# Kernel tuning notes

Measured on AMD Instinct MI355X. Metric: run time of the kernel, lower is better.

Reference implementation:

```python
import jax, jax.numpy as jnp
import numpy as np

EPS = 1e-8  # torch F.cosine_similarity denominator clamp


def setup_inputs() -> dict:
    key = jax.random.key(0)
    k1, k2 = jax.random.split(key)
    N, D = 8192, 256
    return {
        "output1": jax.random.normal(k1, (N, D), dtype=jnp.float32),
        "output2": jax.random.normal(k2, (N, D), dtype=jnp.float32),
    }


def reference(output1, output2):
    N = output2.shape[0]
    # cosine similarity matrix via normalize + GEMM, with torch's eps clamp
    n1 = jnp.linalg.norm(output1, axis=-1, keepdims=True)  # [N,1]
    n2 = jnp.linalg.norm(output2, axis=-1, keepdims=True)  # [N,1]
    dots = output1 @ output2.T  # [N,N]
    denom = jnp.maximum(n1 * n2.T, EPS)
    cos = dots / denom
    # subtract tiny diagonal as in original
    cos = cos - jnp.eye(N, dtype=cos.dtype) * 1e-12
    # cross entropy with labels = arange(N)
    logZ = jax.nn.logsumexp(cos, axis=-1)  # [N]
    diag = jnp.diagonal(cos)  # logits at true label i
    loss = jnp.mean(logZ - diag)
    return loss
```

## Files before the change

### kernel.cpp

```cpp
#include <hip/hip_runtime.h>
#include <hip/hip_bf16.h>

#define N 8192
#define D 256
#define SP 8
#define NCHK 16

typedef __bf16 bf16x8 __attribute__((ext_vector_type(8)));
typedef float f32x4 __attribute__((ext_vector_type(4)));

static __device__ __forceinline__ unsigned short f2bf(float x) {
    union { float f; unsigned int u; } c; c.f = x;
    unsigned int r = (c.u + 0x7fffu + ((c.u >> 16) & 1u)) >> 16;
    return (unsigned short)r;
}

static __device__ __forceinline__ void gll16(const void* g, void* l) {
    __builtin_amdgcn_global_load_lds(
        (const __attribute__((address_space(1))) void*)g,
        (__attribute__((address_space(3))) void*)l, 16, 0, 0);
}

#define WAIT_VM0  asm volatile("s_waitcnt vmcnt(0)" ::: "memory")
#define WAIT_LG0  asm volatile("s_waitcnt lgkmcnt(0)" ::: "memory")
#define SBAR      __builtin_amdgcn_s_barrier()
#define SCHED0    __builtin_amdgcn_sched_barrier(0)

__global__ __launch_bounds__(256) void conv_k(const float* __restrict__ o1,
                                              const float* __restrict__ o2,
                                              unsigned char* __restrict__ a_bf,
                                              unsigned char* __restrict__ b_bf,
                                              float* __restrict__ diag) {
    const int wid = threadIdx.x >> 6, lane = threadIdx.x & 63;
    const int r = blockIdx.x * 4 + wid;
    const float4* p1 = (const float4*)(o1 + (size_t)r * D);
    const float4* p2 = (const float4*)(o2 + (size_t)r * D);
    float4 v1 = p1[lane], v2 = p2[lane];
    float s1 = v1.x*v1.x + v1.y*v1.y + v1.z*v1.z + v1.w*v1.w;
    float s2 = v2.x*v2.x + v2.y*v2.y + v2.z*v2.z + v2.w*v2.w;
    float sd = v1.x*v2.x + v1.y*v2.y + v1.z*v2.z + v1.w*v2.w;
    #pragma unroll
    for (int m = 1; m < 64; m <<= 1) {
        s1 += __shfl_xor(s1, m);
        s2 += __shfl_xor(s2, m);
        sd += __shfl_xor(sd, m);
    }
    float i1 = 1.0f / sqrtf(s1);
    float i2 = 1.0f / sqrtf(s2);
    if (lane == 0) diag[r] = sd * i1 * i2;

    {
        unsigned int lo = (unsigned int)f2bf(v1.x * i1) | ((unsigned int)f2bf(v1.y * i1) << 16);
        unsigned int hi = (unsigned int)f2bf(v1.z * i1) | ((unsigned int)f2bf(v1.w * i1) << 16);
        uint2 q; q.x = lo; q.y = hi;
        *(uint2*)(a_bf + (size_t)r * 512 + lane * 8) = q;
    }
    {
        unsigned int lo = (unsigned int)f2bf(v2.x * i2) | ((unsigned int)f2bf(v2.y * i2) << 16);
        unsigned int hi = (unsigned int)f2bf(v2.z * i2) | ((unsigned int)f2bf(v2.w * i2) << 16);
        int c  = lane >> 1;
        int cs = c ^ (r & 31);
        uint2 q; q.x = lo; q.y = hi;
        *(uint2*)(b_bf + (size_t)r * 512 + cs * 16 + (lane & 1) * 8) = q;
    }
}

__global__ __launch_bounds__(256, 2) void gemm8(const unsigned char* __restrict__ a_bf,
                                                const unsigned char* __restrict__ b_bf,
                                                float* __restrict__ s_part) {
    __shared__ __align__(16) unsigned char bls[2][64 * 512];
    __shared__ float red[2][128];

    const int tid = threadIdx.x;
    const int lane = tid & 63, wid = tid >> 6;
    const int wr = wid >> 1, wc = wid & 1;
    const int l15 = lane & 15, lk = lane >> 4;
    const int bid = blockIdx.x;
    const int sp = bid & 7, rb = bid >> 3;

    const unsigned char* aG = a_bf + (size_t)rb * (128 * 512);
    const unsigned char* bG = b_bf + (size_t)sp * ((size_t)1024 * 512);

    bf16x8 af[4][8];
    #pragma unroll
    for (int mr = 0; mr < 4; ++mr)
        #pragma unroll
        for (int ks = 0; ks < 8; ++ks)
            af[mr][ks] = *(const bf16x8*)(aG + (size_t)(wr * 64 + mr * 16 + l15) * 512
                                             + ks * 64 + lk * 16);

    #pragma unroll
    for (int it = 0; it < 8; ++it) {
        int x = it * 4096 + tid * 16;
        gll16(bG + x, &bls[0][x]);
    }

    float srow[4][4];
    #pragma unroll
    for (int mr = 0; mr < 4; ++mr)
        #pragma unroll
        for (int rg = 0; rg < 4; ++rg) srow[mr][rg] = 0.f;

    const unsigned char* cur = bls[0];
    unsigned char* nxt = bls[1];

    #pragma unroll 1
    for (int p = 0; p < NCHK; ++p) {
        WAIT_VM0;
        SCHED0;
        SBAR;

        if (p < NCHK - 1) {
            const unsigned char* src = bG + (size_t)(p + 1) * 32768;
            #pragma unroll
            for (int it = 0; it < 8; ++it) {
                int x = it * 4096 + tid * 16;
                gll16(src + x, nxt + x);
            }
        }

        f32x4 acc[4][2];
        #pragma unroll
        for (int mr = 0; mr < 4; ++mr)
            #pragma unroll
            for (int nc = 0; nc < 2; ++nc)
                acc[mr][nc] = (f32x4){0.f, 0.f, 0.f, 0.f};

        __builtin_amdgcn_s_setprio(1);
        #pragma unroll
        for (int ks = 0; ks < 8; ++ks) {
            bf16x8 bb[2];
            #pragma unroll
            for (int nc = 0; nc < 2; ++nc) {
                const int col = wc * 32 + nc * 16 + l15;
                const int cs = (ks * 4 + lk) ^ (col & 31);
                bb[nc] = *(const bf16x8*)(cur + col * 512 + cs * 16);
            }
            #pragma unroll
            for (int nc = 0; nc < 2; ++nc)
                #pragma unroll
                for (int mr = 0; mr < 4; ++mr)
                    acc[mr][nc] = __builtin_amdgcn_mfma_f32_16x16x32_bf16(
                        af[mr][ks], bb[nc], acc[mr][nc], 0, 0, 0);
        }
        __builtin_amdgcn_s_setprio(0);
        WAIT_LG0;
        SCHED0;

        #pragma unroll
        for (int mr = 0; mr < 4; ++mr)
            #pragma unroll
            for (int rg = 0; rg < 4; ++rg)
                srow[mr][rg] += __expf(acc[mr][0][rg]) + __expf(acc[mr][1][rg]);

        unsigned char* t = (unsigned char*)cur; cur = nxt; nxt = t;
    }

    #pragma unroll
    for (int mr = 0; mr < 4; ++mr)
        #pragma unroll
        for (int rg = 0; rg < 4; ++rg) {
            float v = srow[mr][rg];
            v += __shfl_xor(v, 1);
            v += __shfl_xor(v, 2);
            v += __shfl_xor(v, 4);
            v += __shfl_xor(v, 8);
            srow[mr][rg] = v;
        }
    if (l15 == 0) {
        #pragma unroll
        for (int mr = 0; mr < 4; ++mr)
            #pragma unroll
            for (int rg = 0; rg < 4; ++rg)
                red[wc][wr * 64 + mr * 16 + lk * 4 + rg] = srow[mr][rg];
    }
    __syncthreads();
    if (tid < 128) {
        s_part[(size_t)sp * N + rb * 128 + tid] = red[0][tid] + red[1][tid];
    }
}

__global__ __launch_bounds__(128) void rowloss3(const float* __restrict__ s_part,
                                                const float* __restrict__ diag,
                                                float* __restrict__ partial) {
    const int t = threadIdx.x, rb = blockIdx.x;
    float s = 0.f;
    #pragma unroll
    for (int sp = 0; sp < SP; ++sp)
        s += s_part[(size_t)sp * N + rb * 128 + t];
    float loss = logf(s) - diag[rb * 128 + t];
    #pragma unroll
    for (int m = 1; m < 64; m <<= 1) loss += __shfl_xor(loss, m);
    __shared__ float redl[2];
    if ((t & 63) == 0) redl[t >> 6] = loss;
    __syncthreads();
    if (t == 0) partial[rb] = redl[0] + redl[1];
}

__global__ __launch_bounds__(64) void final_k(const float* __restrict__ partial,
                                              float* __restrict__ out) {
    const int t = threadIdx.x;
    float v = partial[t];
    #pragma unroll
    for (int m = 1; m < 64; m <<= 1) v += __shfl_xor(v, m);
    if (t == 0) out[0] = v / (float)N;
}

extern "C" void kernel_launch(void* const* d_in, const int* in_sizes, int n_in,
                              void* d_out, int out_size, void* d_ws, size_t ws_size,
                              hipStream_t stream) {
    const float* o1 = (const float*)d_in[0];
    const float* o2 = (const float*)d_in[1];

    unsigned char* w = (unsigned char*)d_ws;
    unsigned char* a_bf = w;
    unsigned char* b_bf = w + (size_t)4 * 1024 * 1024;
    float* diag    = (float*)(w + (size_t)8 * 1024 * 1024);
    float* s_part  = diag + N;
    float* partial = s_part + (size_t)SP * N;

    conv_k<<<N / 4, 256, 0, stream>>>(o1, o2, a_bf, b_bf, diag);
    gemm8<<<512, 256, 0, stream>>>(a_bf, b_bf, s_part);
    rowloss3<<<N / 128, 128, 0, stream>>>(s_part, diag, partial);
    final_k<<<1, 64, 0, stream>>>(partial, (float*)d_out);
}
```

Before: 53.54 us.

## Give each wave private double-buffered B staging and fold log2e into A

The GEMM now has each wave stream its own 16-column B chunks into a private LDS double buffer, waiting with vmcnt(8). This removes the block-wide barrier per chunk, and each wave computes one column group over 32 smaller chunks. The A operand is prescaled by log2(e) in the conversion kernel, so the softmax sum can use exp2f instead of __expf. In exchange, B tiles that two waves used to share are now loaded twice from global memory, which roughly doubles B traffic through L2. Per-chunk MFMA work is also smaller, which exposes more load latency.

```diff
diff --git a/kernel.cpp b/kernel.cpp
--- a/kernel.cpp
+++ b/kernel.cpp
@@ -4,7 +4,8 @@
 #define N 8192
 #define D 256
 #define SP 8
-#define NCHK 16
+#define NCHK 32
+#define LOG2E 1.44269504088896f
 
 typedef __bf16 bf16x8 __attribute__((ext_vector_type(8)));
 typedef float f32x4 __attribute__((ext_vector_type(4)));
@@ -21,9 +22,9 @@
         (__attribute__((address_space(3))) void*)l, 16, 0, 0);
 }
 
+#define WAIT_VM8  asm volatile("s_waitcnt vmcnt(8)" ::: "memory")
 #define WAIT_VM0  asm volatile("s_waitcnt vmcnt(0)" ::: "memory")
 #define WAIT_LG0  asm volatile("s_waitcnt lgkmcnt(0)" ::: "memory")
-#define SBAR      __builtin_amdgcn_s_barrier()
 #define SCHED0    __builtin_amdgcn_sched_barrier(0)
 
 __global__ __launch_bounds__(256) void conv_k(const float* __restrict__ o1,
@@ -49,9 +50,10 @@
     float i2 = 1.0f / sqrtf(s2);
     if (lane == 0) diag[r] = sd * i1 * i2;
 
+    float a_sc = i1 * LOG2E;
     {
-        unsigned int lo = (unsigned int)f2bf(v1.x * i1) | ((unsigned int)f2bf(v1.y * i1) << 16);
-        unsigned int hi = (unsigned int)f2bf(v1.z * i1) | ((unsigned int)f2bf(v1.w * i1) << 16);
+        unsigned int lo = (unsigned int)f2bf(v1.x * a_sc) | ((unsigned int)f2bf(v1.y * a_sc) << 16);
+        unsigned int hi = (unsigned int)f2bf(v1.z * a_sc) | ((unsigned int)f2bf(v1.w * a_sc) << 16);
         uint2 q; q.x = lo; q.y = hi;
         *(uint2*)(a_bf + (size_t)r * 512 + lane * 8) = q;
     }
@@ -65,96 +67,89 @@
     }
 }
 
-__global__ __launch_bounds__(256, 2) void gemm8(const unsigned char* __restrict__ a_bf,
+__global__ __launch_bounds__(256, 2) void gemm9(const unsigned char* __restrict__ a_bf,
                                                 const unsigned char* __restrict__ b_bf,
                                                 float* __restrict__ s_part) {
-    __shared__ __align__(16) unsigned char bls[2][64 * 512];
+    __shared__ __align__(16) unsigned char bls[4][16384];
     __shared__ float red[2][128];
 
     const int tid = threadIdx.x;
     const int lane = tid & 63, wid = tid >> 6;
-    const int wr = wid >> 1, wc = wid & 1;
+    const int wrow = wid >> 1, ch = wid & 1;
     const int l15 = lane & 15, lk = lane >> 4;
     const int bid = blockIdx.x;
-    const int sp = bid & 7, rb = bid >> 3;
-
-    const unsigned char* aG = a_bf + (size_t)rb * (128 * 512);
-    const unsigned char* bG = b_bf + (size_t)sp * ((size_t)1024 * 512);
+    const int panel = bid & 7, rb = bid >> 3;
+
+    const unsigned char* aG = a_bf + (size_t)(rb * 128 + wrow * 64) * 512;
+    const unsigned char* bG = b_bf + (size_t)(panel * 1024 + ch * 512) * 512;
+    unsigned char* myl = bls[wid];
 
     bf16x8 af[4][8];
     #pragma unroll
     for (int mr = 0; mr < 4; ++mr)
         #pragma unroll
         for (int ks = 0; ks < 8; ++ks)
-            af[mr][ks] = *(const bf16x8*)(aG + (size_t)(wr * 64 + mr * 16 + l15) * 512
+            af[mr][ks] = *(const bf16x8*)(aG + (size_t)(mr * 16 + l15) * 512
                                              + ks * 64 + lk * 16);
 
-    #pragma unroll
-    for (int it = 0; it < 8; ++it) {
-        int x = it * 4096 + tid * 16;
-        gll16(bG + x, &bls[0][x]);
-    }
+#define STAGE(c, b)                                                             \
+    {                                                                           \
+        const unsigned char* src_ = bG + (size_t)(c) * 8192;                    \
+        unsigned char* dst_ = myl + (b) * 8192;                                 \
+        _Pragma("unroll")                                                       \
+        for (int it = 0; it < 8; ++it) {                                        \
+            int x_ = it * 1024 + lane * 16;                                     \
+            gll16(src_ + x_, dst_ + x_);                                        \
+        }                                                                       \
+    }
+
+    STAGE(0, 0);
+    STAGE(1, 1);
 
     float srow[4][4];
     #pragma unroll
     for (int mr = 0; mr < 4; ++mr)
         #pragma unroll
         for (int rg = 0; rg < 4; ++rg) srow[mr][rg] = 0.f;
-
-    const unsigned char* cur = bls[0];
-    unsigned char* nxt = bls[1];
 
     #pragma unroll 1
     for (int p = 0; p < NCHK; ++p) {
-        WAIT_VM0;
+        if (p < NCHK - 1) { WAIT_VM8; } else { WAIT_VM0; }
         SCHED0;
-        SBAR;
-
-        if (p < NCHK - 1) {
-            const unsigned char* src = bG + (size_t)(p + 1) * 32768;
-            #pragma unroll
-            for (int it = 0; it < 8; ++it) {
-                int x = it * 4096 + tid * 16;
-                gll16(src + x, nxt + x);
-            }
+
+        const unsigned char* cb = myl + (p & 1) * 8192;
+        const int key = (p & 1) * 16 + l15;
+        bf16x8 bb[8];
+        #pragma unroll
+        for (int ks = 0; ks < 8; ++ks) {
+            const int cs = (ks * 4 + lk) ^ key;
+            bb[ks] = *(const bf16x8*)(cb + l15 * 512 + cs * 16);
         }
-
-        f32x4 acc[4][2];
-        #pragma unroll
-        for (int mr = 0; mr < 4; ++mr)
-            #pragma unroll
-            for (int nc = 0; nc < 2; ++nc)
-                acc[mr][nc] = (f32x4){0.f, 0.f, 0.f, 0.f};
-
-        __builtin_amdgcn_s_setprio(1);
-        #pragma unroll
-        for (int ks = 0; ks < 8; ++ks) {
-            bf16x8 bb[2];
-            #pragma unroll
-            for (int nc = 0; nc < 2; ++nc) {
-                const int col = wc * 32 + nc * 16 + l15;
-                const int cs = (ks * 4 + lk) ^ (col & 31);
-                bb[nc] = *(const bf16x8*)(cur + col * 512 + cs * 16);
-            }
-            #pragma unroll
-            for (int nc = 0; nc < 2; ++nc)
-                #pragma unroll
-                for (int mr = 0; mr < 4; ++mr)
-                    acc[mr][nc] = __builtin_amdgcn_mfma_f32_16x16x32_bf16(
-                        af[mr][ks], bb[nc], acc[mr][nc], 0, 0, 0);
-        }
-        __builtin_amdgcn_s_setprio(0);
         WAIT_LG0;
         SCHED0;
+        if (p + 2 < NCHK) STAGE(p + 2, p & 1);
+        SCHED0;
+
+        f32x4 acc[4];
+        #pragma unroll
+        for (int mr = 0; mr < 4; ++mr) acc[mr] = (f32x4){0.f, 0.f, 0.f, 0.f};
+
+        __builtin_amdgcn_s_setprio(1);
+        #pragma unroll
+        for (int ks = 0; ks < 8; ++ks)
+            #pragma unroll
+            for (int mr = 0; mr < 4; ++mr)
+                acc[mr] = __builtin_amdgcn_mfma_f32_16x16x32_bf16(
+                    af[mr][ks], bb[ks], acc[mr], 0, 0, 0);
+        __builtin_amdgcn_s_setprio(0);
 
         #pragma unroll
         for (int mr = 0; mr < 4; ++mr)
             #pragma unroll
             for (int rg = 0; rg < 4; ++rg)
-                srow[mr][rg] += __expf(acc[mr][0][rg]) + __expf(acc[mr][1][rg]);
-
-        unsigned char* t = (unsigned char*)cur; cur = nxt; nxt = t;
-    }
+                srow[mr][rg] += exp2f(acc[mr][rg]);
+    }
+#undef STAGE
 
     #pragma unroll
     for (int mr = 0; mr < 4; ++mr)
@@ -172,11 +167,11 @@
         for (int mr = 0; mr < 4; ++mr)
             #pragma unroll
             for (int rg = 0; rg < 4; ++rg)
-                red[wc][wr * 64 + mr * 16 + lk * 4 + rg] = srow[mr][rg];
+                red[ch][wrow * 64 + mr * 16 + lk * 4 + rg] = srow[mr][rg];
     }
     __syncthreads();
     if (tid < 128) {
-        s_part[(size_t)sp * N + rb * 128 + tid] = red[0][tid] + red[1][tid];
+        s_part[(size_t)panel * N + rb * 128 + tid] = red[0][tid] + red[1][tid];
     }
 }
 
@@ -220,7 +215,7 @@
     float* partial = s_part + (size_t)SP * N;
 
     conv_k<<<N / 4, 256, 0, stream>>>(o1, o2, a_bf, b_bf, diag);
-    gemm8<<<512, 256, 0, stream>>>(a_bf, b_bf, s_part);
+    gemm9<<<512, 256, 0, stream>>>(a_bf, b_bf, s_part);
     rowloss3<<<N / 128, 128, 0, stream>>>(s_part, diag, partial);
     final_k<<<1, 64, 0, stream>>>(partial, (float*)d_out);
 }
```

Measured after the change: 62.57 us. 1.17x slower.

## Switch similarity GEMM from bf16 to fp8 scaled MFMA with log2e folding

Applied to the files above, without the earlier changes.

Normalized rows are now quantized to fp8 instead of bf16. The GEMM uses the 16x16x128 f8f6f4 scaled MFMA with neutral scales, which halves operand bytes and LDS traffic and cuts the number of MFMA issues. The LDS swizzle is reworked for the 256-byte rows. The log2(e) factor is folded into the A operand so the epilogue can use exp2f instead of expf. The cost is fp8 precision in the cosine logits, which may shift the loss beyond tolerance.

```diff
diff --git a/kernel.cpp b/kernel.cpp
--- a/kernel.cpp
+++ b/kernel.cpp
@@ -5,15 +5,11 @@
 #define D 256
 #define SP 8
 #define NCHK 16
-
-typedef __bf16 bf16x8 __attribute__((ext_vector_type(8)));
+#define LOG2E 1.44269504088896f
+
+typedef int   i32x4 __attribute__((ext_vector_type(4)));
+typedef int   i32x8 __attribute__((ext_vector_type(8)));
 typedef float f32x4 __attribute__((ext_vector_type(4)));
-
-static __device__ __forceinline__ unsigned short f2bf(float x) {
-    union { float f; unsigned int u; } c; c.f = x;
-    unsigned int r = (c.u + 0x7fffu + ((c.u >> 16) & 1u)) >> 16;
-    return (unsigned short)r;
-}
 
 static __device__ __forceinline__ void gll16(const void* g, void* l) {
     __builtin_amdgcn_global_load_lds(
@@ -28,8 +24,8 @@
 
 __global__ __launch_bounds__(256) void conv_k(const float* __restrict__ o1,
                                               const float* __restrict__ o2,
-                                              unsigned char* __restrict__ a_bf,
-                                              unsigned char* __restrict__ b_bf,
+                                              unsigned char* __restrict__ a8,
+                                              unsigned char* __restrict__ b8,
                                               float* __restrict__ diag) {
     const int wid = threadIdx.x >> 6, lane = threadIdx.x & 63;
     const int r = blockIdx.x * 4 + wid;
@@ -49,26 +45,25 @@
     float i2 = 1.0f / sqrtf(s2);
     if (lane == 0) diag[r] = sd * i1 * i2;
 
+    float a_sc = i1 * LOG2E;
     {
-        unsigned int lo = (unsigned int)f2bf(v1.x * i1) | ((unsigned int)f2bf(v1.y * i1) << 16);
-        unsigned int hi = (unsigned int)f2bf(v1.z * i1) | ((unsigned int)f2bf(v1.w * i1) << 16);
-        uint2 q; q.x = lo; q.y = hi;
-        *(uint2*)(a_bf + (size_t)r * 512 + lane * 8) = q;
+        int pa = __builtin_amdgcn_cvt_pk_fp8_f32(v1.x * a_sc, v1.y * a_sc, 0, false);
+        pa     = __builtin_amdgcn_cvt_pk_fp8_f32(v1.z * a_sc, v1.w * a_sc, pa, true);
+        *(int*)(a8 + (size_t)r * 256 + lane * 4) = pa;
     }
     {
-        unsigned int lo = (unsigned int)f2bf(v2.x * i2) | ((unsigned int)f2bf(v2.y * i2) << 16);
-        unsigned int hi = (unsigned int)f2bf(v2.z * i2) | ((unsigned int)f2bf(v2.w * i2) << 16);
-        int c  = lane >> 1;
-        int cs = c ^ (r & 31);
-        uint2 q; q.x = lo; q.y = hi;
-        *(uint2*)(b_bf + (size_t)r * 512 + cs * 16 + (lane & 1) * 8) = q;
-    }
-}
-
-__global__ __launch_bounds__(256, 2) void gemm8(const unsigned char* __restrict__ a_bf,
-                                                const unsigned char* __restrict__ b_bf,
-                                                float* __restrict__ s_part) {
-    __shared__ __align__(16) unsigned char bls[2][64 * 512];
+        int pb = __builtin_amdgcn_cvt_pk_fp8_f32(v2.x * i2, v2.y * i2, 0, false);
+        pb     = __builtin_amdgcn_cvt_pk_fp8_f32(v2.z * i2, v2.w * i2, pb, true);
+        int c  = lane >> 2;
+        int cs = c ^ (r & 15);
+        *(int*)(b8 + (size_t)r * 256 + cs * 16 + (lane & 3) * 4) = pb;
+    }
+}
+
+__global__ __launch_bounds__(256, 2) void gemm11(const unsigned char* __restrict__ a8,
+                                                 const unsigned char* __restrict__ b8,
+                                                 float* __restrict__ s_part) {
+    __shared__ __align__(16) unsigned char bls[2][16384];
     __shared__ float red[2][128];
 
     const int tid = threadIdx.x;
@@ -76,21 +71,21 @@
     const int wr = wid >> 1, wc = wid & 1;
     const int l15 = lane & 15, lk = lane >> 4;
     const int bid = blockIdx.x;
-    const int sp = bid & 7, rb = bid >> 3;
-
-    const unsigned char* aG = a_bf + (size_t)rb * (128 * 512);
-    const unsigned char* bG = b_bf + (size_t)sp * ((size_t)1024 * 512);
-
-    bf16x8 af[4][8];
+    const int panel = bid & 7, rb = bid >> 3;
+
+    const unsigned char* aG = a8 + (size_t)rb * (128 * 256);
+    const unsigned char* bG = b8 + (size_t)panel * ((size_t)1024 * 256);
+
+    i32x8 af[4][2];
     #pragma unroll
     for (int mr = 0; mr < 4; ++mr)
         #pragma unroll
-        for (int ks = 0; ks < 8; ++ks)
-            af[mr][ks] = *(const bf16x8*)(aG + (size_t)(wr * 64 + mr * 16 + l15) * 512
-                                             + ks * 64 + lk * 16);
-
-    #pragma unroll
-    for (int it = 0; it < 8; ++it) {
+        for (int kh = 0; kh < 2; ++kh)
+            af[mr][kh] = *(const i32x8*)(aG + (size_t)(wr * 64 + mr * 16 + l15) * 256
+                                            + kh * 128 + lk * 32);
+
+    #pragma unroll
+    for (int it = 0; it < 4; ++it) {
         int x = it * 4096 + tid * 16;
         gll16(bG + x, &bls[0][x]);
     }
@@ -101,8 +96,7 @@
         #pragma unroll
         for (int rg = 0; rg < 4; ++rg) srow[mr][rg] = 0.f;
 
-    const unsigned char* cur = bls[0];
-    unsigned char* nxt = bls[1];
+    int cur = 0;
 
     #pragma unroll 1
     for (int p = 0; p < NCHK; ++p) {
@@ -111,11 +105,12 @@
         SBAR;
 
         if (p < NCHK - 1) {
-            const unsigned char* src = bG + (size_t)(p + 1) * 32768;
-            #pragma unroll
-            for (int it = 0; it < 8; ++it) {
+            const unsigned char* src = bG + (size_t)(p + 1) * 16384;
+            unsigned char* dst = bls[cur ^ 1];
+            #pragma unroll
+            for (int it = 0; it < 4; ++it) {
                 int x = it * 4096 + tid * 16;
-                gll16(src + x, nxt + x);
+                gll16(src + x, dst + x);
             }
         }
 
@@ -126,22 +121,33 @@
             for (int nc = 0; nc < 2; ++nc)
                 acc[mr][nc] = (f32x4){0.f, 0.f, 0.f, 0.f};
 
+        const unsigned char* cb = bls[cur];
+
         __builtin_amdgcn_s_setprio(1);
         #pragma unroll
-        for (int ks = 0; ks < 8; ++ks) {
-            bf16x8 bb[2];
+        for (int kh = 0; kh < 2; ++kh) {
+            i32x8 bb[2];
             #pragma unroll
             for (int nc = 0; nc < 2; ++nc) {
                 const int col = wc * 32 + nc * 16 + l15;
-                const int cs = (ks * 4 + lk) ^ (col & 31);
-                bb[nc] = *(const bf16x8*)(cur + col * 512 + cs * 16);
+                const int c0  = kh * 8 + lk * 2;
+                const int cs0 = c0 ^ l15;
+                i32x4 lo = *(const i32x4*)(cb + col * 256 + cs0 * 16);
+                i32x4 hi = *(const i32x4*)(cb + col * 256 + (cs0 ^ 1) * 16);
+                i32x8 b;
+                b[0] = lo[0]; b[1] = lo[1]; b[2] = lo[2]; b[3] = lo[3];
+                b[4] = hi[0]; b[5] = hi[1]; b[6] = hi[2]; b[7] = hi[3];
+                bb[nc] = b;
             }
             #pragma unroll
             for (int nc = 0; nc < 2; ++nc)
                 #pragma unroll
                 for (int mr = 0; mr < 4; ++mr)
-                    acc[mr][nc] = __builtin_amdgcn_mfma_f32_16x16x32_bf16(
-                        af[mr][ks], bb[nc], acc[mr][nc], 0, 0, 0);
+                    acc[mr][nc] = __builtin_amdgcn_mfma_scale_f32_16x16x128_f8f6f4(
+                        af[mr][kh], bb[nc], acc[mr][nc],
+                        0, 0,
+                        0, 0x7F,
+                        0, 0x7F);
         }
         __builtin_amdgcn_s_setprio(0);
         WAIT_LG0;
@@ -151,9 +157,9 @@
         for (int mr = 0; mr < 4; ++mr)
             #pragma unroll
             for (int rg = 0; rg < 4; ++rg)
-                srow[mr][rg] += __expf(acc[mr][0][rg]) + __expf(acc[mr][1][rg]);
-
-        unsigned char* t = (unsigned char*)cur; cur = nxt; nxt = t;
+                srow[mr][rg] += exp2f(acc[mr][0][rg]) + exp2f(acc[mr][1][rg]);
+
+        cur ^= 1;
     }
 
     #pragma unroll
@@ -176,7 +182,7 @@
     }
     __syncthreads();
     if (tid < 128) {
-        s_part[(size_t)sp * N + rb * 128 + tid] = red[0][tid] + red[1][tid];
+        s_part[(size_t)panel * N + rb * 128 + tid] = red[0][tid] + red[1][tid];
     }
 }
 
@@ -213,14 +219,14 @@
     const float* o2 = (const float*)d_in[1];
 
     unsigned char* w = (unsigned char*)d_ws;
-    unsigned char* a_bf = w;
-    unsigned char* b_bf = w + (size_t)4 * 1024 * 1024;
-    float* diag    = (float*)(w + (size_t)8 * 1024 * 1024);
+    unsigned char* a8 = w;
+    unsigned char* b8 = w + (size_t)2 * 1024 * 1024;
+    float* diag    = (float*)(w + (size_t)4 * 1024 * 1024);
     float* s_part  = diag + N;
     float* partial = s_part + (size_t)SP * N;
 
-    conv_k<<<N / 4, 256, 0, stream>>>(o1, o2, a_bf, b_bf, diag);
-    gemm8<<<512, 256, 0, stream>>>(a_bf, b_bf, s_part);
+    conv_k<<<N / 4, 256, 0, stream>>>(o1, o2, a8, b8, diag);
+    gemm11<<<512, 256, 0, stream>>>(a8, b8, s_part);
     rowloss3<<<N / 128, 128, 0, stream>>>(s_part, diag, partial);
     final_k<<<1, 64, 0, stream>>>(partial, (float*)d_out);
 }
```

Result: faster. 46.41 us (-13.3%).
